# Performance work log

Hardware: AMD Instinct MI355X
Metric: run time of the kernel (lower is better)

The kernel has to match this reference:

```python
import jax, jax.numpy as jnp
import numpy as np

N_VERTICES = 50000
N_RADIAL = 5
N_ANGULAR = 8
FEATURE_DIM = 64
AMT_TEMPLATES = 64
TEMPLATE_RADIUS = 0.03
ROTATION_DELTA = 1


def create_template_matrix(n_radial, n_angular, radius):
    # Polar grid of template vertices in cartesian coordinates: (R, A, 2)
    radii = radius * (np.arange(1, n_radial + 1) / n_radial)
    angles = 2.0 * np.pi * np.arange(n_angular) / n_angular
    x = radii[:, None] * np.cos(angles)[None, :]
    y = radii[:, None] * np.sin(angles)[None, :]
    return np.stack([x, y], axis=-1).astype(np.float32)


def define_interpolation_coefficients(template_matrix):
    # Gaussian interpolation prior (concrete instance of the abstract method),
    # normalized over all template vertices. Shape: (R, A, R, A)
    R, A, _ = template_matrix.shape
    flat = template_matrix.reshape(R * A, 2)
    d2 = ((flat[:, None, :] - flat[None, :, :]) ** 2).sum(-1)  # (RA, RA)
    sigma = TEMPLATE_RADIUS / N_RADIAL
    w = np.exp(-d2 / (2.0 * sigma ** 2))
    w = w / w.sum(axis=1, keepdims=True)
    return w.reshape(R, A, R, A).astype(np.float32)


def setup_inputs() -> dict:
    key = jax.random.key(0)
    k1, k2, k3, k4, k5, k6, k7 = jax.random.split(key, 7)
    mesh_signal = jax.random.normal(k1, (N_VERTICES, FEATURE_DIM), dtype=jnp.float32)
    # barycentric coordinates: [..., 0] = vertex index (stored as float),
    # [..., 1] = barycentric weight summing to 1 over the 3 triangle corners
    idx = jax.random.randint(k2, (N_VERTICES, N_RADIAL, N_ANGULAR, 3), 0, N_VERTICES)
    w = jax.random.uniform(k3, (N_VERTICES, N_RADIAL, N_ANGULAR, 3), dtype=jnp.float32)
    w = w / jnp.sum(w, axis=-1, keepdims=True)
    bary_coordinates = jnp.stack([idx.astype(jnp.float32), w], axis=-1)
    neighbor_weights = jax.random.normal(
        k4, (AMT_TEMPLATES, N_RADIAL, N_ANGULAR, FEATURE_DIM), dtype=jnp.float32) * 0.05
    center_weights = jax.random.normal(
        k5, (AMT_TEMPLATES, 1, FEATURE_DIM), dtype=jnp.float32) * 0.05
    bias = jax.random.normal(k6, (AMT_TEMPLATES,), dtype=jnp.float32) * 0.05
    tmpl = create_template_matrix(N_RADIAL, N_ANGULAR, TEMPLATE_RADIUS)
    interp_coeff = jnp.asarray(
        define_interpolation_coefficients(tmpl).reshape(N_RADIAL, N_ANGULAR, N_RADIAL * N_ANGULAR))
    return {
        "mesh_signal": mesh_signal,
        "bary_coordinates": bary_coordinates,
        "neighbor_weights": neighbor_weights,
        "center_weights": center_weights,
        "bias": bias,
        "interp_coeff": interp_coeff,
    }


def reference(mesh_signal, bary_coordinates, neighbor_weights, center_weights, bias, interp_coeff):
    N, R, A, _, _ = bary_coordinates.shape
    C = mesh_signal.shape[-1]
    T = neighbor_weights.shape[0]

    # ---- patch operator: barycentric gather + interpolation ----
    idx = bary_coordinates[..., 0].astype(jnp.int32)          # (N, R, A, 3)
    bw = bary_coordinates[..., 1]                              # (N, R, A, 3)
    gathered = mesh_signal[idx]                                # (N, R, A, 3, C)
    interp = jnp.sum(bw[..., None] * gathered, axis=-2)        # (N, R, A, C)

    # ---- prior: matvec with interpolation coefficients ----
    # original: (N,1,1,C,RA) matvec (R,A,RA) -> (N,R,A,C)
    ms = interp.reshape(N, R * A, C)                           # (N, RA, C)
    interp = jnp.einsum('nmc,ram->nrac', ms, interp_coeff)     # (N, R, A, C)

    # ---- center fold: einsum('si,tji->sjt') ----
    conv_center = jnp.einsum('nc,tjc->njt', mesh_signal, center_weights)  # (N, 1, T)

    # ---- neighbor fold over rotations ----
    # roll(interp, shift=r, axis=angular) . W == interp . roll(W, shift=-r, axis=angular)
    rotations = np.arange(0, A, ROTATION_DELTA)
    w_rot = jnp.stack([jnp.roll(neighbor_weights, -int(r), axis=2) for r in rotations])  # (O, T, R, A, C)
    conv_neighbor = jnp.einsum('nrac,otrac->not', interp, w_rot) + bias                  # (N, O, T)

    return jax.nn.relu(conv_center + conv_neighbor)
```

## Files before the change

kernel.cpp:

```cpp
#include <hip/hip_runtime.h>
#include <hip/hip_bf16.h>

#define N_V   50000
#define KTOT  2624
#define NOUT  512
#define NKB   41
#define BM    128
#define BN    256

typedef short v8s __attribute__((ext_vector_type(8)));
typedef float v4f __attribute__((ext_vector_type(4)));
typedef unsigned int v4u __attribute__((ext_vector_type(4)));
typedef unsigned short u16;
typedef unsigned int u32;

__device__ __forceinline__ u16 f2bf(float f) {
    u32 u = __float_as_uint(f);
    return (u16)((u + 0x7FFFu + ((u >> 16) & 1u)) >> 16);
}

__global__ void cast_ms(const float* __restrict__ ms, u16* __restrict__ msb) {
    int i = (blockIdx.x * 256 + threadIdx.x) * 4;
    float4 v = *reinterpret_cast<const float4*>(ms + i);
    ushort4 o;
    o.x = f2bf(v.x); o.y = f2bf(v.y); o.z = f2bf(v.z); o.w = f2bf(v.w);
    *reinterpret_cast<ushort4*>(msb + i) = o;
}

__global__ void build_w2(const float* __restrict__ nw, const float* __restrict__ cw,
                         const float* __restrict__ coeff, u16* __restrict__ w2) {
    int l = blockIdx.x * 256 + threadIdx.x;
    if (l >= NOUT * KTOT) return;
    int j = l / KTOT, k = l - j * KTOT;
    int o = j >> 6, t = j & 63;
    u16 v;
    if (k >= 2560) {
        v = f2bf(cw[t * 64 + (k - 2560)]);
    } else {
        int m = k >> 6, c = k & 63;
        float s = 0.f;
        #pragma unroll
        for (int ra = 0; ra < 40; ++ra) {
            int r = ra >> 3, a = ra & 7;
            s += coeff[ra * 40 + m] * nw[((t * 5 + r) * 8 + ((a + o) & 7)) * 64 + c];
        }
        v = f2bf(s);
    }
    w2[l] = v;
}

__device__ __forceinline__ void gl2lds(const u16* g, u16* l) {
    __builtin_amdgcn_global_load_lds(
        (const __attribute__((address_space(1))) u32*)(uintptr_t)g,
        (__attribute__((address_space(3))) u32*)(uintptr_t)l, 16, 0, 0);
}

__device__ __forceinline__ u32 ipair(u32 pa, u32 pb, u32 pc, float w0, float w1, float w2) {
    float a0 = __uint_as_float(pa << 16), a1 = __uint_as_float(pa & 0xffff0000u);
    float b0 = __uint_as_float(pb << 16), b1 = __uint_as_float(pb & 0xffff0000u);
    float c0 = __uint_as_float(pc << 16), c1 = __uint_as_float(pc & 0xffff0000u);
    float r0 = w0 * a0 + w1 * b0 + w2 * c0;
    float r1 = w0 * a1 + w1 * b1 + w2 * c1;
    return __builtin_amdgcn_perm(__float_as_uint(r1) + 0x8000u,
                                 __float_as_uint(r0) + 0x8000u, 0x07060302u);
}

__global__ __launch_bounds__(512, 2)
void gemm_fused(const float* __restrict__ bary, const u16* __restrict__ msb,
                const u16* __restrict__ w2, const float* __restrict__ bias,
                float* __restrict__ out) {
    __shared__ u16 At[BM * 64];
    __shared__ u16 Bt[2 * BN * 64];

    const int tid  = threadIdx.x;
    const int lane = tid & 63, wave = tid >> 6;
    const int l15  = lane & 15, q = lane >> 4;
    const int wm   = wave >> 2, wn = wave & 3;

    const int id  = blockIdx.x;
    const int bx  = id % 391, by = id / 391;
    const int row0 = bx * BM, col0 = by * BN;

    const int ar  = tid >> 2;
    const u32 acb = (u32)(tid & 3) * 32;
    int an = row0 + ar; if (an > N_V - 1) an = N_V - 1;
    const u32* brow = (const u32*)bary + (size_t)an * 240;
    const u32 an_off = (u32)an * 128 + acb;

    const int e_a = ar & 7;
    const u32 at_w0 = (u32)ar * 128 + (u32)(((2 * (tid & 3)) ^ e_a) * 16);
    const u32 at_w1 = at_w0 ^ 16;

    const int eq = l15 & 7;
    const u32 a_rd0 = (u32)(wm * 64 + l15) * 128 + (u32)((q ^ eq) * 16);
    const u32 b_rd0 = (u32)(wn * 64 + l15) * 128 + (u32)((q ^ eq) * 16);

    const int rl = lane >> 3;
    const int bl = (lane & 7) ^ rl;

    v4f acc[4][4];
    #pragma unroll
    for (int mi = 0; mi < 4; ++mi)
        #pragma unroll
        for (int ni = 0; ni < 4; ++ni)
            acc[mi][ni] = (v4f){0.f, 0.f, 0.f, 0.f};

    v4u G0_0a, G0_0b, G0_1a, G0_1b, G0_2a, G0_2b;
    v4u G1_0a, G1_0b, G1_1a, G1_1b, G1_2a, G1_2b;
    v4u B0lo, B0hi, B1lo, B1hi;
    float w00, w01, w02, w10, w11, w12;
    v4u cv0, cv1;

#define BARY_LOAD(DLO, DHI, kc) do { \
    u32 _d0 = ((u32)((kc) * 6)) & ~3u; \
    DLO = *(const v4u*)(brow + _d0); \
    DHI = *(const v4u*)(brow + _d0 + 4); } while (0)

#define DECODE_ISSUE(PAR, BLO, BHI, Ga0, Gb0, Ga1, Gb1, Ga2, Gb2, W0, W1, W2) do { \
    u32 uf0, uw0, uf1, uw1, uf2, uw2; \
    if (PAR) { uf0 = BLO[2]; uw0 = BLO[3]; uf1 = BHI[0]; uw1 = BHI[1]; uf2 = BHI[2]; uw2 = BHI[3]; } \
    else     { uf0 = BLO[0]; uw0 = BLO[1]; uf1 = BLO[2]; uw1 = BLO[3]; uf2 = BHI[0]; uw2 = BHI[1]; } \
    u32 _o0 = ((u32)(int)__uint_as_float(uf0) << 7) + acb; \
    u32 _o1 = ((u32)(int)__uint_as_float(uf1) << 7) + acb; \
    u32 _o2 = ((u32)(int)__uint_as_float(uf2) << 7) + acb; \
    const char* _mb = (const char*)msb; \
    Ga0 = *(const v4u*)(_mb + _o0); Gb0 = *(const v4u*)(_mb + _o0 + 16); \
    Ga1 = *(const v4u*)(_mb + _o1); Gb1 = *(const v4u*)(_mb + _o1 + 16); \
    Ga2 = *(const v4u*)(_mb + _o2); Gb2 = *(const v4u*)(_mb + _o2 + 16); \
    W0 = __uint_as_float(uw0); W1 = __uint_as_float(uw1); W2 = __uint_as_float(uw2); } while (0)

#define CONVERT(Ga0, Gb0, Ga1, Gb1, Ga2, Gb2, W0, W1, W2) do { \
    _Pragma("unroll") \
    for (int _j = 0; _j < 4; ++_j) { \
        cv0[_j] = ipair(Ga0[_j], Ga1[_j], Ga2[_j], W0, W1, W2); \
        cv1[_j] = ipair(Gb0[_j], Gb1[_j], Gb2[_j], W0, W1, W2); } } while (0)

#define BLDS(KB_LD, BUF) do { \
    _Pragma("unroll") \
    for (int _ii = 0; _ii < 4; ++_ii) { \
        int _we = wave * 4 + _ii; \
        u32 _src = (u32)(col0 + _we * 8 + rl) * KTOT + (u32)(KB_LD) * 64 + (u32)(bl * 8); \
        gl2lds(w2 + _src, &Bt[(BUF) * (BN * 64) + _we * 512]); } } while (0)

#define AT_STORE() do { \
    *(v4u*)((char*)At + at_w0) = cv0; \
    *(v4u*)((char*)At + at_w1) = cv1; } while (0)

#define MFMA_STEP(BUF) do { \
    const char* _atp = (const char*)At; \
    const char* _btp = (const char*)Bt + (BUF) * (BN * 64 * 2); \
    _Pragma("unroll") \
    for (int _s = 0; _s < 2; ++_s) { \
        u32 _ao = a_rd0 ^ (u32)(_s * 64), _bo = b_rd0 ^ (u32)(_s * 64); \
        v8s _af[4], _bf[4]; \
        _Pragma("unroll") \
        for (int _mi = 0; _mi < 4; ++_mi) _af[_mi] = *(const v8s*)(_atp + _ao + _mi * 2048); \
        _Pragma("unroll") \
        for (int _ni = 0; _ni < 4; ++_ni) _bf[_ni] = *(const v8s*)(_btp + _bo + _ni * 2048); \
        _Pragma("unroll") \
        for (int _mi = 0; _mi < 4; ++_mi) \
            _Pragma("unroll") \
            for (int _ni = 0; _ni < 4; ++_ni) \
                acc[_mi][_ni] = __builtin_amdgcn_mfma_f32_16x16x32_bf16( \
                    _af[_mi], _bf[_ni], acc[_mi][_ni], 0, 0, 0); } } while (0)

#define BAR2_12() asm volatile("s_waitcnt vmcnt(12) lgkmcnt(0)\ns_barrier" ::: "memory")
#define BAR2_10() asm volatile("s_waitcnt vmcnt(10) lgkmcnt(0)\ns_barrier" ::: "memory")
#define BAR2_6()  asm volatile("s_waitcnt vmcnt(6) lgkmcnt(0)\ns_barrier"  ::: "memory")
#define BAR2_4()  asm volatile("s_waitcnt vmcnt(4) lgkmcnt(0)\ns_barrier"  ::: "memory")
#define BAR2_0()  asm volatile("s_waitcnt vmcnt(0) lgkmcnt(0)\ns_barrier"  ::: "memory")
#define BAR1()    asm volatile("s_barrier" ::: "memory")

    BARY_LOAD(B0lo, B0hi, 0);
    DECODE_ISSUE(0, B0lo, B0hi, G0_0a, G0_0b, G0_1a, G0_1b, G0_2a, G0_2b, w00, w01, w02);
    BARY_LOAD(B1lo, B1hi, 1);
    DECODE_ISSUE(1, B1lo, B1hi, G1_0a, G1_0b, G1_1a, G1_1b, G1_2a, G1_2b, w10, w11, w12);
    BARY_LOAD(B0lo, B0hi, 2);
    BLDS(0, 0);

    #pragma unroll 1
    for (int i = 0; i < 20; ++i) {
        {
            const int kb = 2 * i;
            CONVERT(G0_0a, G0_0b, G0_1a, G0_1b, G0_2a, G0_2b, w00, w01, w02);
            if (kb <= 36) BARY_LOAD(B1lo, B1hi, kb + 3);
            if (kb <= 37) {
                DECODE_ISSUE(0, B0lo, B0hi, G0_0a, G0_0b, G0_1a, G0_1b, G0_2a, G0_2b,
                             w00, w01, w02);
            } else if (kb == 38) {
                G0_0a = *(const v4u*)((const char*)msb + an_off);
                G0_0b = *(const v4u*)((const char*)msb + an_off + 16);
            }
            BAR1();
            BLDS(kb + 1, 1);
            AT_STORE();
            if (kb <= 36) BAR2_12(); else BAR2_6();
            MFMA_STEP(0);
        }
        {
            const int kb = 2 * i + 1;
            CONVERT(G1_0a, G1_0b, G1_1a, G1_1b, G1_2a, G1_2b, w10, w11, w12);
            if (kb <= 36) BARY_LOAD(B0lo, B0hi, kb + 3);
            if (kb <= 37)
                DECODE_ISSUE(1, B1lo, B1hi, G1_0a, G1_0b, G1_1a, G1_1b, G1_2a, G1_2b,
                             w10, w11, w12);
            BAR1();
            BLDS(kb + 1, 0);
            AT_STORE();
            if (kb <= 36) BAR2_12();
            else if (kb == 37) BAR2_10();
            else BAR2_4();
            MFMA_STEP(1);
        }
    }
    {
        cv0 = G0_0a; cv1 = G0_0b;
        BAR1();
        AT_STORE();
        BAR2_0();
        MFMA_STEP(0);
    }

    float bv[4];
    #pragma unroll
    for (int ni = 0; ni < 4; ++ni) bv[ni] = bias[ni * 16 + l15];
    #pragma unroll
    for (int mi = 0; mi < 4; ++mi) {
        int rbase = row0 + wm * 64 + mi * 16 + q * 4;
        #pragma unroll
        for (int ni = 0; ni < 4; ++ni) {
            int cg = col0 + wn * 64 + ni * 16 + l15;
            #pragma unroll
            for (int rg = 0; rg < 4; ++rg) {
                int rr = rbase + rg;
                if (rr < N_V) {
                    float v = acc[mi][ni][rg] + bv[ni];
                    out[(size_t)rr * NOUT + cg] = v > 0.f ? v : 0.f;
                }
            }
        }
    }
}

extern "C" void kernel_launch(void* const* d_in, const int* in_sizes, int n_in,
                              void* d_out, int out_size, void* d_ws, size_t ws_size,
                              hipStream_t stream) {
    const float* ms    = (const float*)d_in[0];
    const float* bary  = (const float*)d_in[1];
    const float* nw    = (const float*)d_in[2];
    const float* cw    = (const float*)d_in[3];
    const float* bias  = (const float*)d_in[4];
    const float* coeff = (const float*)d_in[5];
    float* out = (float*)d_out;

    u16* msb = (u16*)d_ws;
    u16* w2  = (u16*)((char*)d_ws + 6400000);

    cast_ms<<<3125, 256, 0, stream>>>(ms, msb);
    build_w2<<<(NOUT * KTOT + 255) / 256, 256, 0, stream>>>(nw, cw, coeff, w2);
    gemm_fused<<<782, 512, 0, stream>>>(bary, msb, w2, bias, out);
}
```

Baseline: 462.0 us.

## Split gather-interpolation into separate kernel materializing X before plain GEMM

Instead of doing the barycentric gather and interpolation inside the GEMM's A-tile load, a new build_x kernel writes the full interpolated bf16 activation matrix X (N x 2624) to workspace, and cast_ms also writes the center columns into it. A simpler gemm2 then streams X and W2 via global_load_lds with higher occupancy (4 blocks/SM) and grouped block ordering. This moves irregular gather latency out of the MFMA loop, at the cost of writing and re-reading about 262 MB of intermediate data. The new path runs only when the workspace is large enough, otherwise the old fused path is used.

```diff
diff --git a/kernel.cpp b/kernel.cpp
--- a/kernel.cpp
+++ b/kernel.cpp
@@ -19,12 +19,33 @@
     return (u16)((u + 0x7FFFu + ((u >> 16) & 1u)) >> 16);
 }
 
-__global__ void cast_ms(const float* __restrict__ ms, u16* __restrict__ msb) {
+__device__ __forceinline__ void gl2lds(const u16* g, u16* l) {
+    __builtin_amdgcn_global_load_lds(
+        (const __attribute__((address_space(1))) u32*)(uintptr_t)g,
+        (__attribute__((address_space(3))) u32*)(uintptr_t)l, 16, 0, 0);
+}
+
+__device__ __forceinline__ u32 ipair(u32 pa, u32 pb, u32 pc, float w0, float w1, float w2) {
+    float a0 = __uint_as_float(pa << 16), a1 = __uint_as_float(pa & 0xffff0000u);
+    float b0 = __uint_as_float(pb << 16), b1 = __uint_as_float(pb & 0xffff0000u);
+    float c0 = __uint_as_float(pc << 16), c1 = __uint_as_float(pc & 0xffff0000u);
+    float r0 = w0 * a0 + w1 * b0 + w2 * c0;
+    float r1 = w0 * a1 + w1 * b1 + w2 * c1;
+    return __builtin_amdgcn_perm(__float_as_uint(r1) + 0x8000u,
+                                 __float_as_uint(r0) + 0x8000u, 0x07060302u);
+}
+
+__global__ void cast_ms(const float* __restrict__ ms, u16* __restrict__ msb,
+                        u16* __restrict__ Xc) {
     int i = (blockIdx.x * 256 + threadIdx.x) * 4;
     float4 v = *reinterpret_cast<const float4*>(ms + i);
     ushort4 o;
     o.x = f2bf(v.x); o.y = f2bf(v.y); o.z = f2bf(v.z); o.w = f2bf(v.w);
     *reinterpret_cast<ushort4*>(msb + i) = o;
+    if (Xc) {
+        int n = i >> 6, c = i & 63;
+        *reinterpret_cast<ushort4*>(Xc + (size_t)n * KTOT + 2560 + c) = o;
+    }
 }
 
 __global__ void build_w2(const float* __restrict__ nw, const float* __restrict__ cw,
@@ -49,20 +70,128 @@
     w2[l] = v;
 }
 
-__device__ __forceinline__ void gl2lds(const u16* g, u16* l) {
-    __builtin_amdgcn_global_load_lds(
-        (const __attribute__((address_space(1))) u32*)(uintptr_t)g,
-        (__attribute__((address_space(3))) u32*)(uintptr_t)l, 16, 0, 0);
-}
-
-__device__ __forceinline__ u32 ipair(u32 pa, u32 pb, u32 pc, float w0, float w1, float w2) {
-    float a0 = __uint_as_float(pa << 16), a1 = __uint_as_float(pa & 0xffff0000u);
-    float b0 = __uint_as_float(pb << 16), b1 = __uint_as_float(pb & 0xffff0000u);
-    float c0 = __uint_as_float(pc << 16), c1 = __uint_as_float(pc & 0xffff0000u);
-    float r0 = w0 * a0 + w1 * b0 + w2 * c0;
-    float r1 = w0 * a1 + w1 * b1 + w2 * c1;
-    return __builtin_amdgcn_perm(__float_as_uint(r1) + 0x8000u,
-                                 __float_as_uint(r0) + 0x8000u, 0x07060302u);
+__global__ void build_x(const float* __restrict__ bary, const u16* __restrict__ msb,
+                        u16* __restrict__ X) {
+    u32 t = blockIdx.x * 256 + threadIdx.x;
+    u32 n = t / 160u;
+    u32 rem = t - n * 160u;
+    u32 m = rem >> 2, j = rem & 3;
+    const float* bb = bary + (size_t)n * 240 + m * 6;
+    float2 p0 = *(const float2*)(bb);
+    float2 p1 = *(const float2*)(bb + 2);
+    float2 p2 = *(const float2*)(bb + 4);
+    u32 jb = j * 32u;
+    u32 o0 = ((u32)(int)p0.x) * 128u + jb;
+    u32 o1 = ((u32)(int)p1.x) * 128u + jb;
+    u32 o2 = ((u32)(int)p2.x) * 128u + jb;
+    const char* mb = (const char*)msb;
+    v4u a0 = *(const v4u*)(mb + o0), b0 = *(const v4u*)(mb + o0 + 16);
+    v4u a1 = *(const v4u*)(mb + o1), b1 = *(const v4u*)(mb + o1 + 16);
+    v4u a2 = *(const v4u*)(mb + o2), b2 = *(const v4u*)(mb + o2 + 16);
+    v4u c0, c1;
+    #pragma unroll
+    for (int e = 0; e < 4; ++e) {
+        c0[e] = ipair(a0[e], a1[e], a2[e], p0.y, p1.y, p2.y);
+        c1[e] = ipair(b0[e], b1[e], b2[e], p0.y, p1.y, p2.y);
+    }
+    char* xp = (char*)X + (size_t)n * (KTOT * 2) + m * 128 + jb;
+    *(v4u*)xp = c0;
+    *(v4u*)(xp + 16) = c1;
+}
+
+__global__ __launch_bounds__(512, 4)
+void gemm2(const u16* __restrict__ X, const u16* __restrict__ w2,
+           const float* __restrict__ bias, float* __restrict__ out) {
+    __shared__ u16 At[BM * 64];
+    __shared__ u16 Bt[BN * 64];
+
+    const int tid  = threadIdx.x;
+    const int lane = tid & 63, wave = tid >> 6;
+    const int l15  = lane & 15, q = lane >> 4;
+    const int wm   = wave >> 2, wn = wave & 3;
+
+    const int id = blockIdx.x;
+    const int p  = (id & 7) + 8 * (id >> 4);
+    const int by = (id >> 3) & 1;
+    if (p >= 391) return;
+    const int row0 = p * BM, col0 = by * BN;
+
+    u32 aoff[2];
+    #pragma unroll
+    for (int h = 0; h < 2; ++h) {
+        int slot = wave * 128 + h * 64 + lane;
+        int arow = slot >> 3, ablk = (slot & 7) ^ (arow & 7);
+        int grow = row0 + arow; if (grow > N_V - 1) grow = N_V - 1;
+        aoff[h] = (u32)grow * (u32)KTOT + (u32)(ablk * 8);
+    }
+    u32 boff[4];
+    #pragma unroll
+    for (int i = 0; i < 4; ++i) {
+        int slot = wave * 256 + i * 64 + lane;
+        int brow = slot >> 3, bblk = (slot & 7) ^ (brow & 7);
+        boff[i] = (u32)(col0 + brow) * (u32)KTOT + (u32)(bblk * 8);
+    }
+
+    const int eq = l15 & 7;
+    const u32 a_rd0 = (u32)(wm * 64 + l15) * 128 + (u32)((q ^ eq) * 16);
+    const u32 b_rd0 = (u32)(wn * 64 + l15) * 128 + (u32)((q ^ eq) * 16);
+
+    v4f acc[4][4];
+    #pragma unroll
+    for (int mi = 0; mi < 4; ++mi)
+        #pragma unroll
+        for (int ni = 0; ni < 4; ++ni)
+            acc[mi][ni] = (v4f){0.f, 0.f, 0.f, 0.f};
+
+    #pragma unroll 1
+    for (int kb = 0; kb < NKB; ++kb) {
+        __syncthreads();
+        #pragma unroll
+        for (int h = 0; h < 2; ++h)
+            gl2lds(X + aoff[h] + kb * 64, &At[wave * 1024 + h * 512]);
+        #pragma unroll
+        for (int i = 0; i < 4; ++i)
+            gl2lds(w2 + boff[i] + kb * 64, &Bt[wave * 2048 + i * 512]);
+        __syncthreads();
+
+        const char* atp = (const char*)At;
+        const char* btp = (const char*)Bt;
+        #pragma unroll
+        for (int s = 0; s < 2; ++s) {
+            u32 ao = a_rd0 ^ (u32)(s * 64), bo = b_rd0 ^ (u32)(s * 64);
+            v8s a_f[4], b_f[4];
+            #pragma unroll
+            for (int mi = 0; mi < 4; ++mi) a_f[mi] = *(const v8s*)(atp + ao + mi * 2048);
+            #pragma unroll
+            for (int ni = 0; ni < 4; ++ni) b_f[ni] = *(const v8s*)(btp + bo + ni * 2048);
+            #pragma unroll
+            for (int mi = 0; mi < 4; ++mi)
+                #pragma unroll
+                for (int ni = 0; ni < 4; ++ni)
+                    acc[mi][ni] = __builtin_amdgcn_mfma_f32_16x16x32_bf16(
+                        a_f[mi], b_f[ni], acc[mi][ni], 0, 0, 0);
+        }
+    }
+
+    float bv[4];
+    #pragma unroll
+    for (int ni = 0; ni < 4; ++ni) bv[ni] = bias[ni * 16 + l15];
+    #pragma unroll
+    for (int mi = 0; mi < 4; ++mi) {
+        int rbase = row0 + wm * 64 + mi * 16 + q * 4;
+        #pragma unroll
+        for (int ni = 0; ni < 4; ++ni) {
+            int cg = col0 + wn * 64 + ni * 16 + l15;
+            #pragma unroll
+            for (int rg = 0; rg < 4; ++rg) {
+                int rr = rbase + rg;
+                if (rr < N_V) {
+                    float v = acc[mi][ni][rg] + bv[ni];
+                    out[(size_t)rr * NOUT + cg] = v > 0.f ? v : 0.f;
+                }
+            }
+        }
+    }
 }
 
 __global__ __launch_bounds__(512, 2)
@@ -255,8 +384,18 @@
 
     u16* msb = (u16*)d_ws;
     u16* w2  = (u16*)((char*)d_ws + 6400000);
-
-    cast_ms<<<3125, 256, 0, stream>>>(ms, msb);
-    build_w2<<<(NOUT * KTOT + 255) / 256, 256, 0, stream>>>(nw, cw, coeff, w2);
-    gemm_fused<<<782, 512, 0, stream>>>(bary, msb, w2, bias, out);
-}
+    const size_t x_off  = 9087104;
+    const size_t x_need = x_off + (size_t)N_V * KTOT * 2;
+    u16* X = (u16*)((char*)d_ws + x_off);
+
+    if (ws_size >= x_need) {
+        cast_ms<<<3125, 256, 0, stream>>>(ms, msb, X);
+        build_w2<<<(NOUT * KTOT + 255) / 256, 256, 0, stream>>>(nw, cw, coeff, w2);
+        build_x<<<31250, 256, 0, stream>>>(bary, msb, X);
+        gemm2<<<784, 512, 0, stream>>>(X, w2, bias, out);
+    } else {
+        cast_ms<<<3125, 256, 0, stream>>>(ms, msb, (u16*)nullptr);
+        build_w2<<<(NOUT * KTOT + 255) / 256, 256, 0, stream>>>(nw, cw, coeff, w2);
+        gemm_fused<<<782, 512, 0, stream>>>(bary, msb, w2, bias, out);
+    }
+}
```

Measured after the change: 449.9 us. 2.6% less time.
